# Optimization experiments

Measured on AMD Instinct MI355X. Metric: run time of the kernel, lower is better.

Reference implementation:

```python
import jax, jax.numpy as jnp
import numpy as np

N_QUBITS = 4
DIM = 16
N_QLAYERS = 2

def _cnot_perm(c, t):
    idx = np.arange(DIM)
    cbit = (idx >> (N_QUBITS - 1 - c)) & 1
    return np.where(cbit == 1, idx ^ (1 << (N_QUBITS - 1 - t)), idx)

# ring entanglement: CNOT(0,1), CNOT(1,2), CNOT(2,3), CNOT(3,0)
RING_PERMS = [jnp.asarray(_cnot_perm(i, (i + 1) % N_QUBITS)) for i in range(N_QUBITS)]
_idx = np.arange(DIM)
ZSIGNS = jnp.asarray(np.stack([1.0 - 2.0 * ((_idx >> (N_QUBITS - 1 - q)) & 1) for q in range(N_QUBITS)], axis=1).astype(np.float32))  # (16, 4)

def _rx(t):
    c = jnp.cos(t / 2).astype(jnp.complex64)
    s = jnp.sin(t / 2).astype(jnp.complex64)
    return jnp.stack([jnp.stack([c, -1j * s]), jnp.stack([-1j * s, c])])

def _ry(t):
    c = jnp.cos(t / 2).astype(jnp.complex64)
    s = jnp.sin(t / 2).astype(jnp.complex64)
    return jnp.stack([jnp.stack([c, -s]), jnp.stack([s, c])])

def _rz(t):
    e = jnp.exp(-0.5j * t.astype(jnp.complex64))
    z = jnp.zeros((), jnp.complex64)
    return jnp.stack([jnp.stack([e, z]), jnp.stack([z, jnp.conj(e)])])

def _apply_1q(state, g, q):
    # wire 0 is the most significant bit (PennyLane convention)
    s = state.reshape(2 ** q, 2, 2 ** (N_QUBITS - 1 - q))
    return jnp.einsum('ij,ajc->aic', g, s).reshape(DIM)

def _circuit(angles, qw):
    # angles: (4,), qw: (n_qlayers, 4, 3); returns PauliZ expvals (4,)
    state = jnp.zeros(DIM, jnp.complex64).at[0].set(1.0)
    for q in range(N_QUBITS):
        state = _apply_1q(state, _ry(angles[q]), q)
    for l in range(N_QLAYERS):
        for q in range(N_QUBITS):
            state = _apply_1q(state, _rx(qw[l, q, 0]), q)
            state = _apply_1q(state, _ry(qw[l, q, 1]), q)
            state = _apply_1q(state, _rz(qw[l, q, 2]), q)
        for p in RING_PERMS:
            state = state[p]
    probs = jnp.abs(state) ** 2
    return probs @ ZSIGNS

def _conv(x, w, b, stride, pad):
    y = jax.lax.conv_general_dilated(x, w, (stride, stride), [(pad, pad), (pad, pad)], dimension_numbers=('NCHW', 'OIHW', 'NCHW'))
    return y + b[None, :, None, None]

def _bn(x, g, b, m, v):
    scale = (g / jnp.sqrt(v + 1e-5))[None, :, None, None]
    return (x - m[None, :, None, None]) * scale + b[None, :, None, None]

def _forward(x, c1w, c1b, bn1g, bn1b, bn1m, bn1v, c2w, c2b, bn2g, bn2b, bn2m, bn2v, c3w, c3b, bn3g, bn3b, bn3m, bn3v, pre_w, pre_b, qw, pw1, pb1, pw2, pb2):
    B = x.shape[0]
    h = jax.nn.relu(_bn(_conv(x, c1w, c1b, 4, 3), bn1g, bn1b, bn1m, bn1v))   # (B,32,56,56)
    h = jax.nn.relu(_bn(_conv(h, c2w, c2b, 2, 1), bn2g, bn2b, bn2m, bn2v))   # (B,64,28,28)
    h = jax.nn.relu(_bn(_conv(h, c3w, c3b, 2, 1), bn3g, bn3b, bn3m, bn3v))   # (B,128,14,14)
    h = h.reshape(B, 128, 2, 7, 2, 7).mean(axis=(3, 5))                       # AdaptiveAvgPool2d((2,2))
    f = h.reshape(B, 128 * 4)
    ang = jnp.tanh(f @ pre_w.T + pre_b) * jnp.pi                              # (B,4)
    qout = jax.vmap(lambda a: _circuit(a, qw))(ang)                            # (B,4) batched statevector sim
    h1 = jax.nn.relu(qout @ pw1.T + pb1)                                       # dropout inactive (eval)
    return h1 @ pw2.T + pb2

def setup_inputs() -> dict:
    key = jax.random.key(0)
    ks = jax.random.split(key, 16)
    d = {
        'x': jax.random.normal(ks[0], (128, 3, 224, 224), jnp.float32),
        'c1w': jax.random.normal(ks[1], (32, 3, 7, 7), jnp.float32) * 0.05,
        'c1b': jax.random.normal(ks[2], (32,), jnp.float32) * 0.05,
        'bn1g': jnp.ones((32,), jnp.float32), 'bn1b': jnp.zeros((32,), jnp.float32),
        'bn1m': jnp.zeros((32,), jnp.float32), 'bn1v': jnp.ones((32,), jnp.float32),
        'c2w': jax.random.normal(ks[3], (64, 32, 3, 3), jnp.float32) * 0.05,
        'c2b': jax.random.normal(ks[4], (64,), jnp.float32) * 0.05,
        'bn2g': jnp.ones((64,), jnp.float32), 'bn2b': jnp.zeros((64,), jnp.float32),
        'bn2m': jnp.zeros((64,), jnp.float32), 'bn2v': jnp.ones((64,), jnp.float32),
        'c3w': jax.random.normal(ks[5], (128, 64, 3, 3), jnp.float32) * 0.05,
        'c3b': jax.random.normal(ks[6], (128,), jnp.float32) * 0.05,
        'bn3g': jnp.ones((128,), jnp.float32), 'bn3b': jnp.zeros((128,), jnp.float32),
        'bn3m': jnp.zeros((128,), jnp.float32), 'bn3v': jnp.ones((128,), jnp.float32),
        'pre_w': jax.random.normal(ks[7], (4, 512), jnp.float32) * 0.04,
        'pre_b': jax.random.normal(ks[8], (4,), jnp.float32) * 0.04,
        'qw': jax.random.normal(ks[9], (2, 4, 3), jnp.float32) * 0.1,
        'pw1': jax.random.normal(ks[10], (64, 4), jnp.float32) * 0.5,
        'pb1': jax.random.normal(ks[11], (64,), jnp.float32) * 0.5,
        'pw2': jax.random.normal(ks[12], (5, 64), jnp.float32) * 0.12,
        'pb2': jax.random.normal(ks[13], (5,), jnp.float32) * 0.12,
    }
    return d

def reference(x, c1w, c1b, bn1g, bn1b, bn1m, bn1v, c2w, c2b, bn2g, bn2b, bn2m, bn2v, c3w, c3b, bn3g, bn3b, bn3m, bn3v, pre_w, pre_b, qw, pw1, pb1, pw2, pb2):
    return _forward(x, c1w, c1b, bn1g, bn1b, bn1m, bn1v, c2w, c2b, bn2g, bn2b, bn2m, bn2v, c3w, c3b, bn3g, bn3b, bn3m, bn3v, pre_w, pre_b, qw, pw1, pb1, pw2, pb2)
```

## Files before the change

kernel.cpp:

```cpp
#include <hip/hip_runtime.h>
#include <math.h>

#define DEV __device__ __forceinline__

typedef __attribute__((ext_vector_type(8))) __bf16 bf16x8;
typedef __attribute__((ext_vector_type(4))) float f32x4;

__global__ void prep_weights(
    const float* __restrict__ c1w, const float* __restrict__ c1b,
    const float* __restrict__ g1, const float* __restrict__ b1,
    const float* __restrict__ m1, const float* __restrict__ v1,
    const float* __restrict__ c2w, const float* __restrict__ c2b,
    const float* __restrict__ g2, const float* __restrict__ b2,
    const float* __restrict__ m2, const float* __restrict__ v2,
    const float* __restrict__ c3w, const float* __restrict__ c3b,
    const float* __restrict__ g3, const float* __restrict__ b3,
    const float* __restrict__ m3, const float* __restrict__ v3,
    __bf16* __restrict__ wb1, __bf16* __restrict__ wb2, __bf16* __restrict__ wb3,
    float* __restrict__ sc1, float* __restrict__ sh1,
    float* __restrict__ sc2, float* __restrict__ sh2,
    float* __restrict__ sc3, float* __restrict__ sh3)
{
    int gid = blockIdx.x * 256 + threadIdx.x;
    int gs = gridDim.x * 256;
    for (int e = gid; e < 32 * 192; e += gs) {
        int oc = e / 192, k = e % 192, rr = k >> 3, kw = k & 7;
        wb1[e] = (rr < 21 && kw >= 1) ? (__bf16)c1w[oc * 147 + rr * 7 + kw - 1]
                                      : (__bf16)0.f;
    }
    for (int e = gid; e < 64 * 384; e += gs) {
        int oc = e / 384, k = e % 384, rr = k >> 2, kw = k & 3;
        wb2[e] = (kw >= 1) ? (__bf16)c2w[oc * 288 + rr * 3 + kw - 1] : (__bf16)0.f;
    }
    for (int e = gid; e < 128 * 768; e += gs) {
        int oc = e / 768, k = e % 768, rr = k >> 2, kw = k & 3;
        wb3[e] = (kw >= 1) ? (__bf16)c3w[oc * 576 + rr * 3 + kw - 1] : (__bf16)0.f;
    }
    if (gid < 32) {
        float s = g1[gid] * rsqrtf(v1[gid] + 1e-5f);
        sc1[gid] = s; sh1[gid] = (c1b[gid] - m1[gid]) * s + b1[gid];
    } else if (gid < 96) {
        int i = gid - 32;
        float s = g2[i] * rsqrtf(v2[i] + 1e-5f);
        sc2[i] = s; sh2[i] = (c2b[i] - m2[i]) * s + b2[i];
    } else if (gid < 224) {
        int i = gid - 96;
        float s = g3[i] * rsqrtf(v3[i] + 1e-5f);
        sc3[i] = s; sh3[i] = (c3b[i] - m3[i]) * s + b3[i];
    }
}

__global__ __launch_bounds__(256, 3) void conv1_kernel(
    const float* __restrict__ x,
    const __bf16* __restrict__ wb,
    const float* __restrict__ scale, const float* __restrict__ shift,
    __bf16* __restrict__ out)
{
    constexpr int IHW = 224 * 224, OHW = 56 * 56, LDR = 72;
    __shared__ __attribute__((aligned(16))) __bf16 Is[256 * LDR];
    __shared__ __attribute__((aligned(16))) __bf16 Ws[32 * LDR];

    const int tid = threadIdx.x;
    const int sb0 = blockIdx.x * 256;
    const int sm = tid;

    int a_n, a_ih0, a_iw0;
    {
        int m = sb0 + sm;
        a_n = m / OHW;
        int rem = m % OHW;
        a_ih0 = (rem / 56) * 4 - 3;
        a_iw0 = (rem % 56) * 4 - 3;
    }
    unsigned ihok = 0;
    #pragma unroll
    for (int t = 0; t < 7; ++t)
        ihok |= (unsigned)(((a_ih0 + t) >= 0) && ((a_ih0 + t) < 224)) << t;
    const bool left = (a_iw0 < 0);
    const int boff = a_n * 3 * IHW + a_ih0 * 224 + (a_iw0 - 1);

    const int w_oc = tid >> 3, w_j = tid & 7;
    const int wave = tid >> 6, lane = tid & 63;
    const int quad = lane >> 4, l16 = lane & 15;

    f32x4 acc[2][4] = {};

    float4 RA[8], RB[8];
    bf16x8 wv;

    auto LOADI = [&](int ci) {
        #pragma unroll
        for (int r = 0; r < 8; ++r) {
            const int rr = ci * 8 + r;
            if (rr < 21) {
                const int ic = rr / 7, kh = rr % 7;
                int off = boff + (ic * IHW + kh * 224);
                int o0 = off < 0 ? 0 : off;
                int o1 = (off + 4) < 0 ? 0 : (off + 4);
                RA[r] = *(const float4*)(x + o0);
                RB[r] = *(const float4*)(x + o1);
            }
        }
        wv = *(const bf16x8*)&wb[(size_t)w_oc * 192 + ci * 64 + w_j * 8];
    };

    LOADI(0);

    #pragma unroll
    for (int ci = 0; ci < 3; ++ci) {
        __builtin_amdgcn_s_barrier();
        #pragma unroll
        for (int r = 0; r < 8; ++r) {
            const int rr = ci * 8 + r;
            bf16x8 h;
            if (rr >= 21) {
                h = (bf16x8){};
            } else {
                const int kh = rr % 7;
                float va[8] = {RA[r].x, RA[r].y, RA[r].z, RA[r].w,
                               RB[r].x, RB[r].y, RB[r].z, RB[r].w};
                bool rok = (ihok >> kh) & 1u;
                #pragma unroll
                for (int j = 0; j < 8; ++j) va[j] = rok ? va[j] : 0.f;
                #pragma unroll
                for (int j = 1; j <= 3; ++j) va[j] = left ? 0.f : va[j];
                #pragma unroll
                for (int j = 0; j < 8; ++j) h[j] = (__bf16)va[j];
            }
            *(bf16x8*)&Is[sm * LDR + r * 8] = h;
        }
        *(bf16x8*)&Ws[w_oc * LDR + w_j * 8] = wv;
        if (ci + 1 < 3) LOADI(ci + 1);
        asm volatile("s_waitcnt lgkmcnt(0)" ::: "memory");
        __builtin_amdgcn_s_barrier();

        #pragma unroll
        for (int kk = 0; kk < 2; ++kk) {
            bf16x8 afr[2], bfr[4];
            #pragma unroll
            for (int mt = 0; mt < 2; ++mt)
                afr[mt] = *(const bf16x8*)&Ws[(mt * 16 + l16) * LDR + kk * 32 + quad * 8];
            #pragma unroll
            for (int nt = 0; nt < 4; ++nt)
                bfr[nt] = *(const bf16x8*)&Is[(wave * 64 + nt * 16 + l16) * LDR + kk * 32 + quad * 8];
            #pragma unroll
            for (int mt = 0; mt < 2; ++mt)
                #pragma unroll
                for (int nt = 0; nt < 4; ++nt)
                    acc[mt][nt] = __builtin_amdgcn_mfma_f32_16x16x32_bf16(
                        afr[mt], bfr[nt], acc[mt][nt], 0, 0, 0);
        }
    }

    #pragma unroll
    for (int mt = 0; mt < 2; ++mt) {
        #pragma unroll
        for (int r = 0; r < 4; ++r) {
            int oc = mt * 16 + quad * 4 + r;
            float scl = scale[oc], shf = shift[oc];
            #pragma unroll
            for (int nt = 0; nt < 4; ++nt) {
                int sg = sb0 + wave * 64 + nt * 16 + l16;
                int n = sg / OHW, s = sg % OHW;
                float v = fmaf(acc[mt][nt][r], scl, shf);
                v = v > 0.f ? v : 0.f;
                out[((size_t)n * 32 + oc) * OHW + s] = (__bf16)v;
            }
        }
    }
}

template<int SPB, int WSP, int IC, int IH, int IW, int OH, int OW, int OC,
         int KCH, int GXS>
DEV void conv_bodyB(
    const __bf16* __restrict__ xo,
    const __bf16* __restrict__ wb,
    const float* __restrict__ scale, const float* __restrict__ shift,
    __bf16* __restrict__ out, __bf16* Is, __bf16* Ws)
{
    constexpr int KS = 3, S = 2, P = 1;
    constexpr int KITER = KCH / 64;
    constexpr int OHW = OH * OW, IHW = IH * IW;
    constexpr int LDR = 72;
    constexpr int TPS = 256 / SPB;
    constexpr int RPT = 16 / TPS;
    constexpr int WOC = 4 / WSP;
    constexpr int WLD = (WOC * 32) / 32;
    static_assert(KITER % 2 == 0, "double-buffer needs even KITER");

    const int tid = threadIdx.x;
    int bx = blockIdx.x;
    if (GXS > 0) bx = (bx & 7) * GXS + (bx >> 3);
    const int sb0 = bx * SPB;

    const int s_sp = tid & (SPB - 1);
    const int gbase = (tid / SPB) * RPT;

    int a_n, a_ih0, a_iw0;
    {
        int m = sb0 + s_sp;
        a_n = m / OHW;
        int rem = m % OHW;
        a_ih0 = (rem / OW) * S - P;
        a_iw0 = (rem % OW) * S - P;
    }
    unsigned ihok = 0;
    #pragma unroll
    for (int t = 0; t < KS; ++t)
        ihok |= (unsigned)(((a_ih0 + t) >= 0) && ((a_ih0 + t) < IH)) << t;
    const bool left = (a_iw0 < 0);
    const __bf16* xp = xo + ((size_t)a_n * IC * IHW + (ptrdiff_t)a_ih0 * IW
                             + (a_iw0 - 1));

    const int wave = tid >> 6, lane = tid & 63;
    const int quad = lane >> 4, l16 = lane & 15;
    const int woc = wave / WSP, wsp = wave - woc * WSP;

    f32x4 acc[2][4] = {};

    unsigned PuA[RPT * 2], PuB[RPT * 2];
    bf16x8 wvA[WLD], wvB[WLD];

    auto LOADI = [&](int ci, auto& Pu, auto& wv) {
        const int k0 = ci * 64;
        #pragma unroll
        for (int j = 0; j < RPT; ++j) {
            int rrr = ci * 16 + gbase + j;
            unsigned ic = ((unsigned)rrr * 43691u) >> 17;
            int kh = rrr - (int)ic * 3;
            const unsigned* rp = (const unsigned*)(xp + ((int)ic * IHW + kh * IW));
            Pu[j * 2]     = rp[0];
            Pu[j * 2 + 1] = rp[1];
        }
        #pragma unroll
        for (int i = 0; i < WLD; ++i) {
            int e = i * 256 + tid;
            wv[i] = *(const bf16x8*)&wb[(size_t)(e >> 3) * KCH + k0 + (e & 7) * 8];
        }
    };

    auto STEP = [&](int ci, auto& Pu, auto& wv, auto& Pun, auto& wvn) {
        __builtin_amdgcn_s_barrier();
        #pragma unroll
        for (int q = 0; q < RPT / 2; ++q) {
            union { unsigned u[4]; bf16x8 v; } tm;
            #pragma unroll
            for (int h = 0; h < 2; ++h) {
                const int j = 2 * q + h;
                int rrr = ci * 16 + gbase + j;
                unsigned icq = ((unsigned)rrr * 43691u) >> 17;
                int kh = rrr - (int)icq * 3;
                unsigned t0 = Pu[j * 2], t1 = Pu[j * 2 + 1];
                bool rok = (ihok >> kh) & 1u;
                t0 = rok ? t0 : 0u;
                t1 = rok ? t1 : 0u;
                t0 = left ? (t0 & 0x0000FFFFu) : t0;
                tm.u[h * 2]     = t0;
                tm.u[h * 2 + 1] = t1;
            }
            *(bf16x8*)&Is[s_sp * LDR + (gbase + 2 * q) * 4] = tm.v;
        }
        #pragma unroll
        for (int i = 0; i < WLD; ++i) {
            int e = i * 256 + tid;
            *(bf16x8*)&Ws[(e >> 3) * LDR + (e & 7) * 8] = wv[i];
        }
        asm volatile("s_waitcnt lgkmcnt(0)" ::: "memory");
        __builtin_amdgcn_s_barrier();
        if (ci + 2 < KITER) LOADI(ci + 2, Pun, wvn);

        #pragma unroll
        for (int kk = 0; kk < 2; ++kk) {
            bf16x8 afr[2], bfr[4];
            #pragma unroll
            for (int mt = 0; mt < 2; ++mt)
                afr[mt] = *(const bf16x8*)&Ws[(woc * 32 + mt * 16 + l16) * LDR + kk * 32 + quad * 8];
            #pragma unroll
            for (int nt = 0; nt < 4; ++nt)
                bfr[nt] = *(const bf16x8*)&Is[(wsp * 64 + nt * 16 + l16) * LDR + kk * 32 + quad * 8];
            #pragma unroll
            for (int mt = 0; mt < 2; ++mt)
                #pragma unroll
                for (int nt = 0; nt < 4; ++nt)
                    acc[mt][nt] = __builtin_amdgcn_mfma_f32_16x16x32_bf16(
                        afr[mt], bfr[nt], acc[mt][nt], 0, 0, 0);
        }
    };

    LOADI(0, PuA, wvA);
    LOADI(1, PuB, wvB);
    #pragma unroll
    for (int cc = 0; cc < KITER; cc += 2) {
        STEP(cc,     PuA, wvA, PuA, wvA);
        STEP(cc + 1, PuB, wvB, PuB, wvB);
    }

    #pragma unroll
    for (int mt = 0; mt < 2; ++mt) {
        #pragma unroll
        for (int r = 0; r < 4; ++r) {
            int oc = woc * 32 + mt * 16 + quad * 4 + r;
            float scl = scale[oc], shf = shift[oc];
            #pragma unroll
            for (int nt = 0; nt < 4; ++nt) {
                int sg = sb0 + wsp * 64 + nt * 16 + l16;
                int n = sg / OHW, s = sg % OHW;
                float v = fmaf(acc[mt][nt][r], scl, shf);
                v = v > 0.f ? v : 0.f;
                out[((size_t)n * OC + oc) * OHW + s] = (__bf16)v;
            }
        }
    }
}

__global__ __launch_bounds__(256, 3) void conv2_kernel(
    const __bf16* __restrict__ xo, const __bf16* __restrict__ wb,
    const float* __restrict__ scale, const float* __restrict__ shift,
    __bf16* __restrict__ out)
{
    __shared__ __attribute__((aligned(16))) __bf16 Is[128 * 72];
    __shared__ __attribute__((aligned(16))) __bf16 Ws[64 * 72];
    conv_bodyB<128, 2, 32, 56, 56, 28, 28, 64, 384, 98>(
        xo, wb, scale, shift, out, Is, Ws);
}

__global__ __launch_bounds__(256, 3) void conv3_kernel(
    const __bf16* __restrict__ xo, const __bf16* __restrict__ wb,
    const float* __restrict__ scale, const float* __restrict__ shift,
    __bf16* __restrict__ out)
{
    __shared__ __attribute__((aligned(16))) __bf16 Is[64 * 72];
    __shared__ __attribute__((aligned(16))) __bf16 Ws[128 * 72];
    conv_bodyB<64, 1, 64, 28, 28, 14, 14, 128, 768, 49>(
        xo, wb, scale, shift, out, Is, Ws);
}

__global__ __launch_bounds__(256) void head_kernel(
    const __bf16* __restrict__ c3o,
    const float* __restrict__ pre_w, const float* __restrict__ pre_b,
    const float* __restrict__ qw,
    const float* __restrict__ pw1, const float* __restrict__ pb1,
    const float* __restrict__ pw2, const float* __restrict__ pb2,
    float* __restrict__ out)
{
    __shared__ __attribute__((aligned(16))) __bf16 slab[128 * 196];
    __shared__ float f[512];
    __shared__ float ang[4];
    __shared__ float zexp[4];
    __shared__ float h1[64];

    int b = blockIdx.x;
    int t = threadIdx.x;

    {
        const bf16x8* src = (const bf16x8*)(c3o + (size_t)b * 128 * 196);
        bf16x8* dst = (bf16x8*)slab;
        #pragma unroll
        for (int i = 0; i < 13; ++i) {
            int e = t + i * 256;
            if (e < 3136) dst[e] = src[e];
        }
    }
    __syncthreads();

    for (int p = t; p < 512; p += 256) {
        int c = p >> 2, i = (p >> 1) & 1, j = p & 1;
        int base = c * 196 + (i * 7) * 14 + j * 7;
        float s = 0.f;
        #pragma unroll
        for (int u = 0; u < 7; ++u)
            #pragma unroll
            for (int v = 0; v < 7; ++v)
                s += (float)slab[base + u * 14 + v];
        f[p] = s * (1.f / 49.f);
    }
    __syncthreads();

    int wv = t >> 6, lane = t & 63;
    float partial = 0.f;
    for (int d = lane; d < 512; d += 64)
        partial += f[d] * pre_w[wv * 512 + d];
    #pragma unroll
    for (int off = 32; off > 0; off >>= 1)
        partial += __shfl_down(partial, off, 64);
    if (lane == 0)
        ang[wv] = tanhf(partial + pre_b[wv]) * 3.14159265358979323846f;
    __syncthreads();

    if (t < 16) {
        const int i = t;
        float re = (i == 0) ? 1.f : 0.f;
        float im = 0.f;

        #pragma unroll
        for (int q = 0; q < 4; ++q) {
            const int m = 8 >> q;
            float th = ang[q] * 0.5f;
            float c = cosf(th), s = sinf(th);
            float pr = __shfl_xor(re, m, 64);
            float pi = __shfl_xor(im, m, 64);
            float ts = (i & m) ? s : -s;
            re = c * re + ts * pr;
            im = c * im + ts * pi;
        }
        #pragma unroll
        for (int l = 0; l < 2; ++l) {
            #pragma unroll
            for (int q = 0; q < 4; ++q) {
                const int m = 8 >> q;
                const float* qq = qw + (l * 4 + q) * 3;
                {
                    float th = qq[0] * 0.5f;
                    float c = cosf(th), s = sinf(th);
                    float pr = __shfl_xor(re, m, 64);
                    float pi = __shfl_xor(im, m, 64);
                    float rn = c * re + s * pi;
                    im = c * im - s * pr;
                    re = rn;
                }
                {
                    float th = qq[1] * 0.5f;
                    float c = cosf(th), s = sinf(th);
                    float pr = __shfl_xor(re, m, 64);
                    float pi = __shfl_xor(im, m, 64);
                    float ts = (i & m) ? s : -s;
                    re = c * re + ts * pr;
                    im = c * im + ts * pi;
                }
                {
                    float th = qq[2] * 0.5f;
                    float c = cosf(th), s = sinf(th);
                    float ts = (i & m) ? s : -s;
                    float rn = c * re - ts * im;
                    im = c * im + ts * re;
                    re = rn;
                }
            }
            #pragma unroll
            for (int e = 0; e < 4; ++e) {
                const int cm = 8 >> e, tm = 8 >> ((e + 1) & 3);
                float pr = __shfl_xor(re, tm, 64);
                float pi = __shfl_xor(im, tm, 64);
                bool sw = (i & cm) != 0;
                re = sw ? pr : re;
                im = sw ? pi : im;
            }
        }
        float p2 = re * re + im * im;
        #pragma unroll
        for (int q = 0; q < 4; ++q) {
            const int m = 8 >> q;
            float v = (i & m) ? -p2 : p2;
            v += __shfl_xor(v, 1, 64);
            v += __shfl_xor(v, 2, 64);
            v += __shfl_xor(v, 4, 64);
            v += __shfl_xor(v, 8, 64);
            if (i == 0) zexp[q] = v;
        }
    }
    __syncthreads();

    if (t < 64) {
        float s = pb1[t];
        #pragma unroll
        for (int k = 0; k < 4; ++k) s += zexp[k] * pw1[t * 4 + k];
        h1[t] = s > 0.f ? s : 0.f;
    }
    __syncthreads();

    if (t < 5) {
        float s = pb2[t];
        for (int k = 0; k < 64; ++k) s += h1[k] * pw2[t * 64 + k];
        out[b * 5 + t] = s;
    }
}

extern "C" void kernel_launch(void* const* d_in, const int* in_sizes, int n_in,
                              void* d_out, int out_size, void* d_ws, size_t ws_size,
                              hipStream_t stream) {
    const float* x    = (const float*)d_in[0];
    const float* c1w  = (const float*)d_in[1];
    const float* c1b  = (const float*)d_in[2];
    const float* bn1g = (const float*)d_in[3];
    const float* bn1b = (const float*)d_in[4];
    const float* bn1m = (const float*)d_in[5];
    const float* bn1v = (const float*)d_in[6];
    const float* c2w  = (const float*)d_in[7];
    const float* c2b  = (const float*)d_in[8];
    const float* bn2g = (const float*)d_in[9];
    const float* bn2b = (const float*)d_in[10];
    const float* bn2m = (const float*)d_in[11];
    const float* bn2v = (const float*)d_in[12];
    const float* c3w  = (const float*)d_in[13];
    const float* c3bi = (const float*)d_in[14];
    const float* bn3g = (const float*)d_in[15];
    const float* bn3b = (const float*)d_in[16];
    const float* bn3m = (const float*)d_in[17];
    const float* bn3v = (const float*)d_in[18];
    const float* prw  = (const float*)d_in[19];
    const float* prb  = (const float*)d_in[20];
    const float* qw   = (const float*)d_in[21];
    const float* pw1  = (const float*)d_in[22];
    const float* pb1  = (const float*)d_in[23];
    const float* pw2  = (const float*)d_in[24];
    const float* pb2  = (const float*)d_in[25];

    const int N = in_sizes[0] / (3 * 224 * 224);
    const size_t NC1 = (size_t)N * 32 * 56 * 56;
    const size_t NC2 = (size_t)N * 64 * 28 * 28;
    const size_t NC3 = (size_t)N * 128 * 14 * 14;

    __bf16* ws_h = (__bf16*)d_ws;
    __bf16* c1o = ws_h + 64;
    __bf16* c2o = ws_h + 64 + NC1 + 64 + 64;
    __bf16* c3o = ws_h + 64 + NC1 + 64 + 64 + NC2 + 64;
    __bf16* wb1 = c3o + NC3;
    __bf16* wb2 = wb1 + 32 * 192;
    __bf16* wb3 = wb2 + 64 * 384;
    float* sc1 = (float*)(wb3 + 128 * 768);
    float* sh1 = sc1 + 32;
    float* sc2 = sh1 + 32;  float* sh2 = sc2 + 64;
    float* sc3 = sh2 + 64;  float* sh3 = sc3 + 128;

    prep_weights<<<192, 256, 0, stream>>>(
        c1w, c1b, bn1g, bn1b, bn1m, bn1v,
        c2w, c2b, bn2g, bn2b, bn2m, bn2v,
        c3w, c3bi, bn3g, bn3b, bn3m, bn3v,
        wb1, wb2, wb3, sc1, sh1, sc2, sh2, sc3, sh3);

    conv1_kernel<<<dim3(401408 / 256, 1), 256, 0, stream>>>(x, wb1, sc1, sh1, c1o);
    conv2_kernel<<<dim3(784, 1), 256, 0, stream>>>(c1o, wb2, sc2, sh2, c2o);
    conv3_kernel<<<dim3(392, 1), 256, 0, stream>>>(c2o, wb3, sc3, sh3, c3o);
    head_kernel<<<N, 256, 0, stream>>>(c3o, prw, prb, qw,
                                       pw1, pb1, pw2, pb2, (float*)d_out);
}
```

Before: 223.6 us.

## Halve spatial tile per block in all convs to raise occupancy and grid size

Each conv kernel now processes half as many output positions per block: conv1 uses 128 positions split across two thread groups loading four kernel rows each, and conv2/conv3 use a generalized body parameterized by per-wave M/N tile counts. Smaller per-thread accumulators and register arrays plus higher launch bounds aim for more resident waves and more blocks to hide memory latency. In exchange, each weight tile is reused across fewer spatial positions, so weight traffic and per-block overhead go up.

```diff
diff --git a/kernel.cpp b/kernel.cpp
--- a/kernel.cpp
+++ b/kernel.cpp
@@ -50,23 +50,24 @@
     }
 }
 
-__global__ __launch_bounds__(256, 3) void conv1_kernel(
+__global__ __launch_bounds__(256, 5) void conv1_kernel(
     const float* __restrict__ x,
     const __bf16* __restrict__ wb,
     const float* __restrict__ scale, const float* __restrict__ shift,
     __bf16* __restrict__ out)
 {
     constexpr int IHW = 224 * 224, OHW = 56 * 56, LDR = 72;
-    __shared__ __attribute__((aligned(16))) __bf16 Is[256 * LDR];
+    __shared__ __attribute__((aligned(16))) __bf16 Is[128 * LDR];
     __shared__ __attribute__((aligned(16))) __bf16 Ws[32 * LDR];
 
     const int tid = threadIdx.x;
-    const int sb0 = blockIdx.x * 256;
-    const int sm = tid;
+    const int sb0 = blockIdx.x * 128;
+    const int s_sp = tid & 127;
+    const int grp  = tid >> 7;
 
     int a_n, a_ih0, a_iw0;
     {
-        int m = sb0 + sm;
+        int m = sb0 + s_sp;
         a_n = m / OHW;
         int rem = m % OHW;
         a_ih0 = (rem / 56) * 4 - 3;
@@ -82,24 +83,25 @@
     const int w_oc = tid >> 3, w_j = tid & 7;
     const int wave = tid >> 6, lane = tid & 63;
     const int quad = lane >> 4, l16 = lane & 15;
-
-    f32x4 acc[2][4] = {};
-
-    float4 RA[8], RB[8];
+    const int woc = wave >> 1, wsp = wave & 1;
+
+    f32x4 acc[4] = {};
+
+    float4 RA[4], RB[4];
     bf16x8 wv;
 
     auto LOADI = [&](int ci) {
         #pragma unroll
-        for (int r = 0; r < 8; ++r) {
-            const int rr = ci * 8 + r;
-            if (rr < 21) {
-                const int ic = rr / 7, kh = rr % 7;
-                int off = boff + (ic * IHW + kh * 224);
-                int o0 = off < 0 ? 0 : off;
-                int o1 = (off + 4) < 0 ? 0 : (off + 4);
-                RA[r] = *(const float4*)(x + o0);
-                RB[r] = *(const float4*)(x + o1);
-            }
+        for (int j = 0; j < 4; ++j) {
+            int rr = ci * 8 + grp * 4 + j;
+            unsigned ic = ((unsigned)rr * 37u) >> 8;
+            int kh = rr - (int)ic * 7;
+            bool ld = rr < 21;
+            int off = boff + (int)ic * IHW + kh * 224;
+            int o0 = (!ld || off < 0) ? 0 : off;
+            int o1 = (!ld || (off + 4) < 0) ? 0 : (off + 4);
+            RA[j] = *(const float4*)(x + o0);
+            RB[j] = *(const float4*)(x + o1);
         }
         wv = *(const bf16x8*)&wb[(size_t)w_oc * 192 + ci * 64 + w_j * 8];
     };
@@ -110,24 +112,21 @@
     for (int ci = 0; ci < 3; ++ci) {
         __builtin_amdgcn_s_barrier();
         #pragma unroll
-        for (int r = 0; r < 8; ++r) {
-            const int rr = ci * 8 + r;
+        for (int j = 0; j < 4; ++j) {
+            int rr = ci * 8 + grp * 4 + j;
+            unsigned ic = ((unsigned)rr * 37u) >> 8;
+            int kh = rr - (int)ic * 7;
+            bool live = (rr < 21) && ((ihok >> kh) & 1u);
+            float va[8] = {RA[j].x, RA[j].y, RA[j].z, RA[j].w,
+                           RB[j].x, RB[j].y, RB[j].z, RB[j].w};
+            #pragma unroll
+            for (int u = 0; u < 8; ++u) va[u] = live ? va[u] : 0.f;
+            #pragma unroll
+            for (int u = 1; u <= 3; ++u) va[u] = left ? 0.f : va[u];
             bf16x8 h;
-            if (rr >= 21) {
-                h = (bf16x8){};
-            } else {
-                const int kh = rr % 7;
-                float va[8] = {RA[r].x, RA[r].y, RA[r].z, RA[r].w,
-                               RB[r].x, RB[r].y, RB[r].z, RB[r].w};
-                bool rok = (ihok >> kh) & 1u;
-                #pragma unroll
-                for (int j = 0; j < 8; ++j) va[j] = rok ? va[j] : 0.f;
-                #pragma unroll
-                for (int j = 1; j <= 3; ++j) va[j] = left ? 0.f : va[j];
-                #pragma unroll
-                for (int j = 0; j < 8; ++j) h[j] = (__bf16)va[j];
-            }
-            *(bf16x8*)&Is[sm * LDR + r * 8] = h;
+            #pragma unroll
+            for (int u = 0; u < 8; ++u) h[u] = (__bf16)va[u];
+            *(bf16x8*)&Is[s_sp * LDR + (grp * 4 + j) * 8] = h;
         }
         *(bf16x8*)&Ws[w_oc * LDR + w_j * 8] = wv;
         if (ci + 1 < 3) LOADI(ci + 1);
@@ -136,43 +135,36 @@
 
         #pragma unroll
         for (int kk = 0; kk < 2; ++kk) {
-            bf16x8 afr[2], bfr[4];
-            #pragma unroll
-            for (int mt = 0; mt < 2; ++mt)
-                afr[mt] = *(const bf16x8*)&Ws[(mt * 16 + l16) * LDR + kk * 32 + quad * 8];
+            bf16x8 afr, bfr[4];
+            afr = *(const bf16x8*)&Ws[(woc * 16 + l16) * LDR + kk * 32 + quad * 8];
             #pragma unroll
             for (int nt = 0; nt < 4; ++nt)
-                bfr[nt] = *(const bf16x8*)&Is[(wave * 64 + nt * 16 + l16) * LDR + kk * 32 + quad * 8];
-            #pragma unroll
-            for (int mt = 0; mt < 2; ++mt)
-                #pragma unroll
-                for (int nt = 0; nt < 4; ++nt)
-                    acc[mt][nt] = __builtin_amdgcn_mfma_f32_16x16x32_bf16(
-                        afr[mt], bfr[nt], acc[mt][nt], 0, 0, 0);
-        }
-    }
-
-    #pragma unroll
-    for (int mt = 0; mt < 2; ++mt) {
-        #pragma unroll
-        for (int r = 0; r < 4; ++r) {
-            int oc = mt * 16 + quad * 4 + r;
-            float scl = scale[oc], shf = shift[oc];
-            #pragma unroll
-            for (int nt = 0; nt < 4; ++nt) {
-                int sg = sb0 + wave * 64 + nt * 16 + l16;
-                int n = sg / OHW, s = sg % OHW;
-                float v = fmaf(acc[mt][nt][r], scl, shf);
-                v = v > 0.f ? v : 0.f;
-                out[((size_t)n * 32 + oc) * OHW + s] = (__bf16)v;
-            }
-        }
-    }
-}
-
-template<int SPB, int WSP, int IC, int IH, int IW, int OH, int OW, int OC,
-         int KCH, int GXS>
-DEV void conv_bodyB(
+                bfr[nt] = *(const bf16x8*)&Is[(wsp * 64 + nt * 16 + l16) * LDR + kk * 32 + quad * 8];
+            #pragma unroll
+            for (int nt = 0; nt < 4; ++nt)
+                acc[nt] = __builtin_amdgcn_mfma_f32_16x16x32_bf16(
+                    afr, bfr[nt], acc[nt], 0, 0, 0);
+        }
+    }
+
+    #pragma unroll
+    for (int r = 0; r < 4; ++r) {
+        int oc = woc * 16 + quad * 4 + r;
+        float scl = scale[oc], shf = shift[oc];
+        #pragma unroll
+        for (int nt = 0; nt < 4; ++nt) {
+            int sg = sb0 + wsp * 64 + nt * 16 + l16;
+            int n = sg / OHW, s = sg % OHW;
+            float v = fmaf(acc[nt][r], scl, shf);
+            v = v > 0.f ? v : 0.f;
+            out[((size_t)n * 32 + oc) * OHW + s] = (__bf16)v;
+        }
+    }
+}
+
+template<int SPB, int OCB, int MT, int NT, int IC, int IH, int IW,
+         int OH, int OW, int OC, int KCH, int GXS>
+DEV void conv_bodyC(
     const __bf16* __restrict__ xo,
     const __bf16* __restrict__ wb,
     const float* __restrict__ scale, const float* __restrict__ shift,
@@ -184,8 +176,10 @@
     constexpr int LDR = 72;
     constexpr int TPS = 256 / SPB;
     constexpr int RPT = 16 / TPS;
-    constexpr int WOC = 4 / WSP;
-    constexpr int WLD = (WOC * 32) / 32;
+    constexpr int WSP = SPB / (16 * NT);
+    constexpr int WOC = OCB / (16 * MT);
+    static_assert(WOC * WSP == 4, "wave decomposition");
+    constexpr int WLD = (OCB * 8) / 256;
     static_assert(KITER % 2 == 0, "double-buffer needs even KITER");
 
     const int tid = threadIdx.x;
@@ -214,9 +208,9 @@
 
     const int wave = tid >> 6, lane = tid & 63;
     const int quad = lane >> 4, l16 = lane & 15;
-    const int woc = wave / WSP, wsp = wave - woc * WSP;
-
-    f32x4 acc[2][4] = {};
+    const int woc = wave / WSP, wsp = wave % WSP;
+
+    f32x4 acc[MT][NT] = {};
 
     unsigned PuA[RPT * 2], PuB[RPT * 2];
     bf16x8 wvA[WLD], wvB[WLD];
@@ -271,17 +265,17 @@
 
         #pragma unroll
         for (int kk = 0; kk < 2; ++kk) {
-            bf16x8 afr[2], bfr[4];
-            #pragma unroll
-            for (int mt = 0; mt < 2; ++mt)
-                afr[mt] = *(const bf16x8*)&Ws[(woc * 32 + mt * 16 + l16) * LDR + kk * 32 + quad * 8];
-            #pragma unroll
-            for (int nt = 0; nt < 4; ++nt)
-                bfr[nt] = *(const bf16x8*)&Is[(wsp * 64 + nt * 16 + l16) * LDR + kk * 32 + quad * 8];
-            #pragma unroll
-            for (int mt = 0; mt < 2; ++mt)
+            bf16x8 afr[MT], bfr[NT];
+            #pragma unroll
+            for (int mt = 0; mt < MT; ++mt)
+                afr[mt] = *(const bf16x8*)&Ws[(woc * MT * 16 + mt * 16 + l16) * LDR + kk * 32 + quad * 8];
+            #pragma unroll
+            for (int nt = 0; nt < NT; ++nt)
+                bfr[nt] = *(const bf16x8*)&Is[(wsp * NT * 16 + nt * 16 + l16) * LDR + kk * 32 + quad * 8];
+            #pragma unroll
+            for (int mt = 0; mt < MT; ++mt)
                 #pragma unroll
-                for (int nt = 0; nt < 4; ++nt)
+                for (int nt = 0; nt < NT; ++nt)
                     acc[mt][nt] = __builtin_amdgcn_mfma_f32_16x16x32_bf16(
                         afr[mt], bfr[nt], acc[mt][nt], 0, 0, 0);
         }
@@ -296,14 +290,14 @@
     }
 
     #pragma unroll
-    for (int mt = 0; mt < 2; ++mt) {
+    for (int mt = 0; mt < MT; ++mt) {
         #pragma unroll
         for (int r = 0; r < 4; ++r) {
-            int oc = woc * 32 + mt * 16 + quad * 4 + r;
+            int oc = woc * MT * 16 + mt * 16 + quad * 4 + r;
             float scl = scale[oc], shf = shift[oc];
             #pragma unroll
-            for (int nt = 0; nt < 4; ++nt) {
-                int sg = sb0 + wsp * 64 + nt * 16 + l16;
+            for (int nt = 0; nt < NT; ++nt) {
+                int sg = sb0 + wsp * NT * 16 + nt * 16 + l16;
                 int n = sg / OHW, s = sg % OHW;
                 float v = fmaf(acc[mt][nt][r], scl, shf);
                 v = v > 0.f ? v : 0.f;
@@ -313,25 +307,25 @@
     }
 }
 
-__global__ __launch_bounds__(256, 3) void conv2_kernel(
-    const __bf16* __restrict__ xo, const __bf16* __restrict__ wb,
-    const float* __restrict__ scale, const float* __restrict__ shift,
-    __bf16* __restrict__ out)
-{
-    __shared__ __attribute__((aligned(16))) __bf16 Is[128 * 72];
-    __shared__ __attribute__((aligned(16))) __bf16 Ws[64 * 72];
-    conv_bodyB<128, 2, 32, 56, 56, 28, 28, 64, 384, 98>(
-        xo, wb, scale, shift, out, Is, Ws);
-}
-
-__global__ __launch_bounds__(256, 3) void conv3_kernel(
+__global__ __launch_bounds__(256, 5) void conv2_kernel(
     const __bf16* __restrict__ xo, const __bf16* __restrict__ wb,
     const float* __restrict__ scale, const float* __restrict__ shift,
     __bf16* __restrict__ out)
 {
     __shared__ __attribute__((aligned(16))) __bf16 Is[64 * 72];
+    __shared__ __attribute__((aligned(16))) __bf16 Ws[64 * 72];
+    conv_bodyC<64, 64, 1, 4, 32, 56, 56, 28, 28, 64, 384, 196>(
+        xo, wb, scale, shift, out, Is, Ws);
+}
+
+__global__ __launch_bounds__(256, 4) void conv3_kernel(
+    const __bf16* __restrict__ xo, const __bf16* __restrict__ wb,
+    const float* __restrict__ scale, const float* __restrict__ shift,
+    __bf16* __restrict__ out)
+{
+    __shared__ __attribute__((aligned(16))) __bf16 Is[32 * 72];
     __shared__ __attribute__((aligned(16))) __bf16 Ws[128 * 72];
-    conv_bodyB<64, 1, 64, 28, 28, 14, 14, 128, 768, 49>(
+    conv_bodyC<32, 128, 2, 2, 64, 28, 28, 14, 14, 128, 768, 98>(
         xo, wb, scale, shift, out, Is, Ws);
 }
 
@@ -528,9 +522,9 @@
         c3w, c3bi, bn3g, bn3b, bn3m, bn3v,
         wb1, wb2, wb3, sc1, sh1, sc2, sh2, sc3, sh3);
 
-    conv1_kernel<<<dim3(401408 / 256, 1), 256, 0, stream>>>(x, wb1, sc1, sh1, c1o);
-    conv2_kernel<<<dim3(784, 1), 256, 0, stream>>>(c1o, wb2, sc2, sh2, c2o);
-    conv3_kernel<<<dim3(392, 1), 256, 0, stream>>>(c2o, wb3, sc3, sh3, c3o);
+    conv1_kernel<<<dim3(401408 / 128, 1), 256, 0, stream>>>(x, wb1, sc1, sh1, c1o);
+    conv2_kernel<<<dim3(1568, 1), 256, 0, stream>>>(c1o, wb2, sc2, sh2, c2o);
+    conv3_kernel<<<dim3(784, 1), 256, 0, stream>>>(c2o, wb3, sc3, sh3, c3o);
     head_kernel<<<N, 256, 0, stream>>>(c3o, prw, prb, qw,
                                        pw1, pb1, pw2, pb2, (float*)d_out);
 }
```

Result: no change. 220.4 us (-1.4%).
